# Kernel tuning notes

Hardware: AMD Instinct MI355X
Metric: run time of the kernel (lower is better)

The kernel has to match this reference:

```python
import jax, jax.numpy as jnp
import numpy as np

B, W, LOCAL, GLOBAL = 32, 16, 64, 64
EMB, HIDDEN, OUT, NLAYERS = 256, 512, 64, 3
T = 128  # output_len


def setup_inputs() -> dict:
    key = jax.random.key(0)
    ks = jax.random.split(key, 16)
    s = 0.05
    inp = {
        "z_t": jax.random.normal(ks[0], (B, W, LOCAL), jnp.float32),
        "z_g": jax.random.normal(ks[1], (B, GLOBAL), jnp.float32),
        # embedding: Linear(local+global -> 256, bias=False), torch layout (out,in)
        "w_emb": jax.random.normal(ks[2], (EMB, LOCAL + GLOBAL), jnp.float32) * s,
        # GRU(input_size=1, hidden=256); input is all-zeros so w_ih contributes
        # nothing (only its bias b_ih matters) -> faithfully omit w_ih.
        "gru_w_hh": jax.random.normal(ks[3], (3 * EMB, EMB), jnp.float32) * s,
        "gru_b_ih": jax.random.normal(ks[4], (3 * EMB,), jnp.float32) * s,
        "gru_b_hh": jax.random.normal(ks[5], (3 * EMB,), jnp.float32) * s,
        "mlp_w1": jax.random.normal(ks[6], (HIDDEN, EMB), jnp.float32) * s,
        "mlp_b1": jax.random.normal(ks[7], (HIDDEN,), jnp.float32) * s,
        "mlp_w2": jax.random.normal(ks[8], (HIDDEN, HIDDEN), jnp.float32) * s,
        "mlp_b2": jax.random.normal(ks[9], (HIDDEN,), jnp.float32) * s,
        "mlp_w3": jax.random.normal(ks[10], (HIDDEN, HIDDEN), jnp.float32) * s,
        "mlp_b3": jax.random.normal(ks[11], (HIDDEN,), jnp.float32) * s,
        "mu_w": jax.random.normal(ks[12], (OUT, HIDDEN), jnp.float32) * s,
        "mu_b": jax.random.normal(ks[13], (OUT,), jnp.float32) * s,
        "output_len": T,
    }
    return inp


def _gru_zero_input(h0, w_hh, b_ih, b_hh, length):
    # PyTorch GRU cell with x_t == 0: input-to-hidden term reduces to b_ih.
    b_ir, b_iz, b_in = jnp.split(b_ih, 3)

    def step(h, _):
        gh = h @ w_hh.T + b_hh              # (BW, 3*EMB)
        g_r, g_z, g_n = jnp.split(gh, 3, axis=-1)
        r = jax.nn.sigmoid(b_ir + g_r)
        z = jax.nn.sigmoid(b_iz + g_z)
        n = jnp.tanh(b_in + r * g_n)
        h_new = (1.0 - z) * n + z * h
        return h_new, h_new

    _, hs = jax.lax.scan(step, h0, None, length=length)
    return hs  # (T, BW, EMB)


def reference(z_t, z_g, w_emb, gru_w_hh, gru_b_ih, gru_b_hh,
              mlp_w1, mlp_b1, mlp_w2, mlp_b2, mlp_w3, mlp_b3,
              mu_w, mu_b, output_len):
    b, nw, _ = z_t.shape
    z = jnp.concatenate(
        [z_t, jnp.broadcast_to(z_g[:, None, :], (b, nw, z_g.shape[-1]))], axis=-1)
    emb = z @ w_emb.T                        # (B, W, EMB)
    h0 = emb.reshape(b * nw, -1)             # (BW, EMB) initial hidden state

    hs = _gru_zero_input(h0, gru_w_hh, gru_b_ih, gru_b_hh, output_len)
    h_t = jnp.transpose(hs, (1, 0, 2))       # (BW, T, EMB), batch_first

    # MLP: Linear+ELU (Dropout p=0.05 is identity in eval)
    h = jax.nn.elu(h_t @ mlp_w1.T + mlp_b1)
    h = jax.nn.elu(h @ mlp_w2.T + mlp_b2)
    h = jax.nn.elu(h @ mlp_w3.T + mlp_b3)
    x_mean = h @ mu_w.T + mu_b               # (BW, T, OUT)
    return x_mean.reshape(b, nw * output_len, -1)
```

## Files before the change

### kernel.cpp

```cpp
#include <hip/hip_runtime.h>
#include <hip/hip_bf16.h>


typedef __bf16 bf16_t;
typedef __bf16 bf16x2 __attribute__((ext_vector_type(2)));
typedef __bf16 bf16x4 __attribute__((ext_vector_type(4)));
typedef __bf16 bf16x8 __attribute__((ext_vector_type(8)));
typedef float f32x4 __attribute__((ext_vector_type(4)));

#define MFMA16(a, b, c) __builtin_amdgcn_mfma_f32_16x16x32_bf16(a, b, c, 0, 0, 0)

#define EMB 256
#define TSTEPS 128
#define OUTD 64

#define HS_OFF   0u
#define H0_OFF   33554432u
#define WHH_OFF  34078720u
#define W1_OFF   34471936u
#define W2_OFF   34734080u
#define W3_OFF   35258368u
#define MUW_OFF  35782656u

__device__ __forceinline__ float rcpf(float x){ return __builtin_amdgcn_rcpf(x); }
__device__ __forceinline__ void lds_barrier() {
  asm volatile("s_waitcnt lgkmcnt(0)\n\ts_barrier" ::: "memory");
}
__device__ __forceinline__ float eluf(float x) {
  return (x > 0.f) ? x : (__expf(x) - 1.f);
}

template<int KC>
__device__ __forceinline__ void conv_frag(
    const float* __restrict__ src, bf16_t* __restrict__ dst,
    int NK, int g, int G)
{
  const int K = KC * 128;
  for (int i = g; i < NK; i += G) {
    const int e    = i & 7;
    const int lane = (i >> 3) & 63;
    const int kk   = (i >> 9) & 3;
    const int rem  = i >> 11;
    const int kc   = rem & (KC - 1);
    const int nt   = rem / KC;
    const int l15  = lane & 15, quad = lane >> 4;
    dst[i] = (bf16_t)src[(size_t)(nt * 16 + l15) * K + kc * 128 + kk * 32 + quad * 8 + e];
  }
}

__global__ __launch_bounds__(256) void convert_kernel(
    const float* __restrict__ whh, const float* __restrict__ w1,
    const float* __restrict__ w2, const float* __restrict__ w3,
    const float* __restrict__ muw, char* __restrict__ ws)
{
  const int g = blockIdx.x * 256 + threadIdx.x;
  const int G = gridDim.x * 256;
  bf16_t* d;
  d = (bf16_t*)(ws + WHH_OFF); for (int i = g; i < 196608; i += G) d[i] = (bf16_t)whh[i];
  conv_frag<2>(w1,  (bf16_t*)(ws + W1_OFF),  131072, g, G);
  conv_frag<4>(w2,  (bf16_t*)(ws + W2_OFF),  262144, g, G);
  conv_frag<4>(w3,  (bf16_t*)(ws + W3_OFF),  262144, g, G);
  conv_frag<4>(muw, (bf16_t*)(ws + MUW_OFF), 32768,  g, G);
}

__global__ __launch_bounds__(256) void emb_kernel(
    const float* __restrict__ z_t, const float* __restrict__ z_g,
    const float* __restrict__ w_emb, float* __restrict__ h0)
{
  __shared__ float zrow[128];
  const int bw = blockIdx.x, tid = threadIdx.x;
  if (tid < 128)
    zrow[tid] = (tid < 64) ? z_t[bw * 64 + tid] : z_g[(bw >> 4) * 64 + (tid - 64)];
  __syncthreads();
  const float4* wp = reinterpret_cast<const float4*>(w_emb + (size_t)tid * 128);
  float s = 0.f;
#pragma unroll
  for (int k4 = 0; k4 < 32; ++k4) {
    const float4 w = wp[k4];
    s += zrow[k4 * 4 + 0] * w.x + zrow[k4 * 4 + 1] * w.y
       + zrow[k4 * 4 + 2] * w.z + zrow[k4 * 4 + 3] * w.w;
  }
  h0[(size_t)bw * 256 + tid] = s;
}

__global__ __launch_bounds__(512, 2) void gru_kernel(
    const float* __restrict__ h0, const bf16_t* __restrict__ w_hh,
    const float* __restrict__ b_ih, const float* __restrict__ b_hh,
    bf16_t* __restrict__ hs)
{
  __shared__ __align__(16) bf16_t h16[2][16][264];

  const int tid  = threadIdx.x;
  const int wv   = tid >> 6;
  const int lane = tid & 63;
  const int l15  = lane & 15;
  const int quad = lane >> 4;
  const int bw0  = blockIdx.x * 4;
  const int cA   = wv * 32 + l15;

  bf16x8 wf[6][8];
#pragma unroll
  for (int g = 0; g < 3; ++g)
#pragma unroll
    for (int s = 0; s < 2; ++s) {
      const int n = g * 256 + cA + s * 16;
#pragma unroll
      for (int kk = 0; kk < 8; ++kk)
        wf[g * 2 + s][kk] = *reinterpret_cast<const bf16x8*>(
            w_hh + (size_t)n * 256 + kk * 32 + quad * 8);
    }

  float br[2], bz[2], bin[2], bhn[2], hm[2];
#pragma unroll
  for (int s = 0; s < 2; ++s) {
    const int c = cA + s * 16;
    br[s]  = b_ih[c]       + b_hh[c];
    bz[s]  = b_ih[256 + c] + b_hh[256 + c];
    bin[s] = b_ih[512 + c];
    bhn[s] = b_hh[512 + c];
    hm[s]  = h0[(size_t)(bw0 + quad) * 256 + c];
  }

  {
    bf16x8 zv;
#pragma unroll
    for (int e = 0; e < 8; ++e) zv[e] = (bf16_t)0.f;
    for (int i = tid; i < 1056; i += 512)
      reinterpret_cast<bf16x8*>(h16)[i] = zv;
  }
  __syncthreads();
#pragma unroll
  for (int s = 0; s < 2; ++s)
    h16[0][quad * 4][cA + s * 16] = (bf16_t)hm[s];
  __syncthreads();

  bf16_t* hsp = hs + ((size_t)(bw0 + quad) * TSTEPS) * EMB + cA;

#pragma unroll 1
  for (int t = 0; t < TSTEPS; ++t) {
    const bf16_t (*hr)[264] = h16[t & 1];
    bf16_t (*hw)[264] = h16[(t & 1) ^ 1];

    f32x4 acc[6] = {};
#pragma unroll
    for (int kk = 0; kk < 8; ++kk) {
      const bf16x8 a = *reinterpret_cast<const bf16x8*>(&hr[l15][kk * 32 + quad * 8]);
#pragma unroll
      for (int ct = 0; ct < 6; ++ct)
        acc[ct] = MFMA16(a, wf[ct][kk], acc[ct]);
    }

#pragma unroll
    for (int s = 0; s < 2; ++s) {
      const float gr = acc[s][0]     + br[s];
      const float gz = acc[2 + s][0] + bz[s];
      const float gn = acc[4 + s][0] + bhn[s];
      const float rr = rcpf(1.f + __expf(-gr));
      const float zz = rcpf(1.f + __expf(-gz));
      const float pre = bin[s] + rr * gn;
      const float nn = 1.f - 2.f * rcpf(__expf(2.f * pre) + 1.f);
      hm[s] = nn + zz * (hm[s] - nn);
      const bf16_t nh = (bf16_t)hm[s];
      hw[quad * 4][cA + s * 16] = nh;
      hsp[(size_t)t * EMB + s * 16] = nh;
    }
    lds_barrier();
  }
}

template<int KC>
__device__ __forceinline__ void mlp_layer(
    const bf16_t* __restrict__ Wf, const float* __restrict__ bias,
    bf16_t (*act)[520], int wv, int lane, int l15, int quad)
{
  constexpr int NIT = KC * 4;
  f32x4 acc[8][4] = {};
  bf16x8 wf[2][8];

#pragma unroll
  for (int ct = 0; ct < 8; ++ct)
    wf[0][ct] = *reinterpret_cast<const bf16x8*>(
        Wf + (((size_t)(wv * 8 + ct) * KC) << 11) + lane * 8);

#pragma unroll
  for (int it = 0; it < NIT; ++it) {
    const int cur = it & 1, nxt = cur ^ 1;
    if (it + 1 < NIT) {
      const int kc1 = (it + 1) >> 2, kk1 = (it + 1) & 3;
#pragma unroll
      for (int ct = 0; ct < 8; ++ct)
        wf[nxt][ct] = *reinterpret_cast<const bf16x8*>(
            Wf + ((((size_t)(wv * 8 + ct) * KC + kc1) * 4 + kk1) << 9) + lane * 8);
    }
    const int kc = it >> 2, kk = it & 3;
    bf16x8 a8[4];
#pragma unroll
    for (int mt = 0; mt < 4; ++mt)
      a8[mt] = *reinterpret_cast<const bf16x8*>(
          &act[mt * 16 + l15][kc * 128 + kk * 32 + quad * 8]);
#pragma unroll
    for (int mt = 0; mt < 4; ++mt)
#pragma unroll
      for (int ct = 0; ct < 8; ++ct)
        acc[ct][mt] = MFMA16(wf[cur][ct], a8[mt], acc[ct][mt]);
  }

  __syncthreads();
#pragma unroll
  for (int ct = 0; ct < 8; ++ct) {
    const int nb = (wv * 8 + ct) * 16 + quad * 4;
    const float4 b4 = *reinterpret_cast<const float4*>(bias + nb);
#pragma unroll
    for (int mt = 0; mt < 4; ++mt) {
      bf16x4 v;
      v[0] = (bf16_t)eluf(acc[ct][mt][0] + b4.x);
      v[1] = (bf16_t)eluf(acc[ct][mt][1] + b4.y);
      v[2] = (bf16_t)eluf(acc[ct][mt][2] + b4.z);
      v[3] = (bf16_t)eluf(acc[ct][mt][3] + b4.w);
      *reinterpret_cast<bf16x4*>(&act[mt * 16 + l15][nb]) = v;
    }
  }
  __syncthreads();
}

__global__ __launch_bounds__(256, 2) void mlp_kernel(
    const bf16_t* __restrict__ hs,
    const bf16_t* __restrict__ w1, const float* __restrict__ b1,
    const bf16_t* __restrict__ w2, const float* __restrict__ b2,
    const bf16_t* __restrict__ w3, const float* __restrict__ b3,
    const bf16_t* __restrict__ muw, const float* __restrict__ mub,
    float* __restrict__ out)
{
  __shared__ __align__(16) bf16_t act[64][520];

  const int tid  = threadIdx.x;
  const int wv   = tid >> 6;
  const int lane = tid & 63;
  const int l15  = lane & 15;
  const int quad = lane >> 4;
  const size_t r0 = (size_t)blockIdx.x * 64;

  for (int v = tid; v < 64 * 32; v += 256) {
    const int rr = v >> 5, cc = v & 31;
    bf16x8 x = *reinterpret_cast<const bf16x8*>(hs + (r0 + rr) * EMB + cc * 8);
    *reinterpret_cast<bf16x8*>(&act[rr][cc * 8]) = x;
  }
  __syncthreads();

  mlp_layer<2>(w1, b1, act, wv, lane, l15, quad);
  mlp_layer<4>(w2, b2, act, wv, lane, l15, quad);
  mlp_layer<4>(w3, b3, act, wv, lane, l15, quad);

  f32x4 macc[4] = {};
#pragma unroll
  for (int it = 0; it < 16; ++it) {
    const int kc = it >> 2, kk = it & 3;
    bf16x8 wfm = *reinterpret_cast<const bf16x8*>(
        muw + ((((size_t)wv * 4 + kc) * 4 + kk) << 9) + lane * 8);
#pragma unroll
    for (int i = 0; i < 4; ++i) {
      bf16x8 a = *reinterpret_cast<const bf16x8*>(
          &act[i * 16 + l15][kc * 128 + kk * 32 + quad * 8]);
      macc[i] = MFMA16(wfm, a, macc[i]);
    }
  }
  const int nb = wv * 16 + quad * 4;
  const float4 mb4 = *reinterpret_cast<const float4*>(mub + nb);
#pragma unroll
  for (int i = 0; i < 4; ++i) {
    float4 o;
    o.x = macc[i][0] + mb4.x;
    o.y = macc[i][1] + mb4.y;
    o.z = macc[i][2] + mb4.z;
    o.w = macc[i][3] + mb4.w;
    *reinterpret_cast<float4*>(out + (r0 + i * 16 + l15) * OUTD + nb) = o;
  }
}

extern "C" void kernel_launch(void* const* d_in, const int* in_sizes, int n_in,
                              void* d_out, int out_size, void* d_ws, size_t ws_size,
                              hipStream_t stream) {
  char* ws = (char*)d_ws;

  convert_kernel<<<256, 256, 0, stream>>>(
      (const float*)d_in[3], (const float*)d_in[6], (const float*)d_in[8],
      (const float*)d_in[10], (const float*)d_in[12], ws);

  emb_kernel<<<512, 256, 0, stream>>>(
      (const float*)d_in[0], (const float*)d_in[1], (const float*)d_in[2],
      (float*)(ws + H0_OFF));

  gru_kernel<<<128, 512, 0, stream>>>(
      (const float*)(ws + H0_OFF), (const bf16_t*)(ws + WHH_OFF),
      (const float*)d_in[4], (const float*)d_in[5],
      (bf16_t*)(ws + HS_OFF));

  mlp_kernel<<<1024, 256, 0, stream>>>(
      (const bf16_t*)(ws + HS_OFF),
      (const bf16_t*)(ws + W1_OFF), (const float*)d_in[7],
      (const bf16_t*)(ws + W2_OFF), (const float*)d_in[9],
      (const bf16_t*)(ws + W3_OFF), (const float*)d_in[11],
      (const bf16_t*)(ws + MUW_OFF), (const float*)d_in[13],
      (float*)d_out);
}
```

Measured before the change: 334.3 us.

## Fuse embedding and weight conversion kernels, vectorize conversion, pad GRU LDS rows

Merges the embedding and weight-conversion kernels into one launch: the first 512 blocks compute the embedding and the remaining 256 convert weights. Conversion now handles eight elements per thread with float4 loads and bf16x8 stores instead of scalar element copies. The GRU shared-memory row pitch grows from 264 to 272 elements to change the LDS bank mapping. The output projection swaps its MFMA operands and writes scalar outputs instead of float4, which may reduce store coalescing.

After: 322.7 us. 1.04x faster.

```diff
diff --git a/kernel.cpp b/kernel.cpp
--- a/kernel.cpp
+++ b/kernel.cpp
@@ -29,58 +29,67 @@
 __device__ __forceinline__ float eluf(float x) {
   return (x > 0.f) ? x : (__expf(x) - 1.f);
 }
-
-template<int KC>
-__device__ __forceinline__ void conv_frag(
+__device__ __forceinline__ bf16x8 cvt8(const float* __restrict__ s) {
+  const float4 a = *reinterpret_cast<const float4*>(s);
+  const float4 b = *reinterpret_cast<const float4*>(s + 4);
+  bf16x8 v;
+  v[0] = (bf16_t)a.x; v[1] = (bf16_t)a.y; v[2] = (bf16_t)a.z; v[3] = (bf16_t)a.w;
+  v[4] = (bf16_t)b.x; v[5] = (bf16_t)b.y; v[6] = (bf16_t)b.z; v[7] = (bf16_t)b.w;
+  return v;
+}
+
+template<int KC, int LOGKC>
+__device__ __forceinline__ void conv_frag8(
     const float* __restrict__ src, bf16_t* __restrict__ dst,
-    int NK, int g, int G)
+    int NK8, int g, int G)
 {
   const int K = KC * 128;
-  for (int i = g; i < NK; i += G) {
-    const int e    = i & 7;
-    const int lane = (i >> 3) & 63;
-    const int kk   = (i >> 9) & 3;
-    const int rem  = i >> 11;
+  for (int i8 = g; i8 < NK8; i8 += G) {
+    const int l15  = i8 & 15;
+    const int quad = (i8 >> 4) & 3;
+    const int kk   = (i8 >> 6) & 3;
+    const int rem  = i8 >> 8;
     const int kc   = rem & (KC - 1);
-    const int nt   = rem / KC;
-    const int l15  = lane & 15, quad = lane >> 4;
-    dst[i] = (bf16_t)src[(size_t)(nt * 16 + l15) * K + kc * 128 + kk * 32 + quad * 8 + e];
-  }
-}
-
-__global__ __launch_bounds__(256) void convert_kernel(
+    const int nt   = rem >> LOGKC;
+    *reinterpret_cast<bf16x8*>(dst + (size_t)i8 * 8) =
+        cvt8(src + (size_t)(nt * 16 + l15) * K + kc * 128 + kk * 32 + quad * 8);
+  }
+}
+
+__global__ __launch_bounds__(256) void ce_kernel(
+    const float* __restrict__ z_t, const float* __restrict__ z_g,
+    const float* __restrict__ w_emb, float* __restrict__ h0,
     const float* __restrict__ whh, const float* __restrict__ w1,
     const float* __restrict__ w2, const float* __restrict__ w3,
     const float* __restrict__ muw, char* __restrict__ ws)
 {
-  const int g = blockIdx.x * 256 + threadIdx.x;
-  const int G = gridDim.x * 256;
-  bf16_t* d;
-  d = (bf16_t*)(ws + WHH_OFF); for (int i = g; i < 196608; i += G) d[i] = (bf16_t)whh[i];
-  conv_frag<2>(w1,  (bf16_t*)(ws + W1_OFF),  131072, g, G);
-  conv_frag<4>(w2,  (bf16_t*)(ws + W2_OFF),  262144, g, G);
-  conv_frag<4>(w3,  (bf16_t*)(ws + W3_OFF),  262144, g, G);
-  conv_frag<4>(muw, (bf16_t*)(ws + MUW_OFF), 32768,  g, G);
-}
-
-__global__ __launch_bounds__(256) void emb_kernel(
-    const float* __restrict__ z_t, const float* __restrict__ z_g,
-    const float* __restrict__ w_emb, float* __restrict__ h0)
-{
-  __shared__ float zrow[128];
-  const int bw = blockIdx.x, tid = threadIdx.x;
-  if (tid < 128)
-    zrow[tid] = (tid < 64) ? z_t[bw * 64 + tid] : z_g[(bw >> 4) * 64 + (tid - 64)];
-  __syncthreads();
-  const float4* wp = reinterpret_cast<const float4*>(w_emb + (size_t)tid * 128);
-  float s = 0.f;
-#pragma unroll
-  for (int k4 = 0; k4 < 32; ++k4) {
-    const float4 w = wp[k4];
-    s += zrow[k4 * 4 + 0] * w.x + zrow[k4 * 4 + 1] * w.y
-       + zrow[k4 * 4 + 2] * w.z + zrow[k4 * 4 + 3] * w.w;
-  }
-  h0[(size_t)bw * 256 + tid] = s;
+  const int tid = threadIdx.x;
+  if (blockIdx.x < 512) {
+    __shared__ float zrow[128];
+    const int bw = blockIdx.x;
+    if (tid < 128)
+      zrow[tid] = (tid < 64) ? z_t[bw * 64 + tid] : z_g[(bw >> 4) * 64 + (tid - 64)];
+    __syncthreads();
+    const float4* wp = reinterpret_cast<const float4*>(w_emb + (size_t)tid * 128);
+    float s = 0.f;
+#pragma unroll
+    for (int k4 = 0; k4 < 32; ++k4) {
+      const float4 w = wp[k4];
+      s += zrow[k4 * 4 + 0] * w.x + zrow[k4 * 4 + 1] * w.y
+         + zrow[k4 * 4 + 2] * w.z + zrow[k4 * 4 + 3] * w.w;
+    }
+    h0[(size_t)bw * 256 + tid] = s;
+  } else {
+    const int g = (blockIdx.x - 512) * 256 + tid;
+    const int G = 256 * 256;
+    bf16_t* d = (bf16_t*)(ws + WHH_OFF);
+    for (int i8 = g; i8 < 24576; i8 += G)
+      *reinterpret_cast<bf16x8*>(d + (size_t)i8 * 8) = cvt8(whh + (size_t)i8 * 8);
+    conv_frag8<2, 1>(w1,  (bf16_t*)(ws + W1_OFF),  16384, g, G);
+    conv_frag8<4, 2>(w2,  (bf16_t*)(ws + W2_OFF),  32768, g, G);
+    conv_frag8<4, 2>(w3,  (bf16_t*)(ws + W3_OFF),  32768, g, G);
+    conv_frag8<4, 2>(muw, (bf16_t*)(ws + MUW_OFF),  4096, g, G);
+  }
 }
 
 __global__ __launch_bounds__(512, 2) void gru_kernel(
@@ -88,7 +97,7 @@
     const float* __restrict__ b_ih, const float* __restrict__ b_hh,
     bf16_t* __restrict__ hs)
 {
-  __shared__ __align__(16) bf16_t h16[2][16][264];
+  __shared__ __align__(16) bf16_t h16[2][16][272];
 
   const int tid  = threadIdx.x;
   const int wv   = tid >> 6;
@@ -125,7 +134,7 @@
     bf16x8 zv;
 #pragma unroll
     for (int e = 0; e < 8; ++e) zv[e] = (bf16_t)0.f;
-    for (int i = tid; i < 1056; i += 512)
+    for (int i = tid; i < 1088; i += 512)
       reinterpret_cast<bf16x8*>(h16)[i] = zv;
   }
   __syncthreads();
@@ -138,8 +147,8 @@
 
 #pragma unroll 1
   for (int t = 0; t < TSTEPS; ++t) {
-    const bf16_t (*hr)[264] = h16[t & 1];
-    bf16_t (*hw)[264] = h16[(t & 1) ^ 1];
+    const bf16_t (*hr)[272] = h16[t & 1];
+    bf16_t (*hw)[272] = h16[(t & 1) ^ 1];
 
     f32x4 acc[6] = {};
 #pragma unroll
@@ -252,6 +261,7 @@
   mlp_layer<4>(w3, b3, act, wv, lane, l15, quad);
 
   f32x4 macc[4] = {};
+  const int n = wv * 16 + l15;
 #pragma unroll
   for (int it = 0; it < 16; ++it) {
     const int kc = it >> 2, kk = it & 3;
@@ -261,20 +271,15 @@
     for (int i = 0; i < 4; ++i) {
       bf16x8 a = *reinterpret_cast<const bf16x8*>(
           &act[i * 16 + l15][kc * 128 + kk * 32 + quad * 8]);
-      macc[i] = MFMA16(wfm, a, macc[i]);
-    }
-  }
-  const int nb = wv * 16 + quad * 4;
-  const float4 mb4 = *reinterpret_cast<const float4*>(mub + nb);
-#pragma unroll
-  for (int i = 0; i < 4; ++i) {
-    float4 o;
-    o.x = macc[i][0] + mb4.x;
-    o.y = macc[i][1] + mb4.y;
-    o.z = macc[i][2] + mb4.z;
-    o.w = macc[i][3] + mb4.w;
-    *reinterpret_cast<float4*>(out + (r0 + i * 16 + l15) * OUTD + nb) = o;
-  }
+      macc[i] = MFMA16(a, wfm, macc[i]);
+    }
+  }
+  const float mb = mub[n];
+#pragma unroll
+  for (int i = 0; i < 4; ++i)
+#pragma unroll
+    for (int r = 0; r < 4; ++r)
+      out[(r0 + i * 16 + quad * 4 + r) * OUTD + n] = macc[i][r] + mb;
 }
 
 extern "C" void kernel_launch(void* const* d_in, const int* in_sizes, int n_in,
@@ -282,13 +287,11 @@
                               hipStream_t stream) {
   char* ws = (char*)d_ws;
 
-  convert_kernel<<<256, 256, 0, stream>>>(
+  ce_kernel<<<768, 256, 0, stream>>>(
+      (const float*)d_in[0], (const float*)d_in[1], (const float*)d_in[2],
+      (float*)(ws + H0_OFF),
       (const float*)d_in[3], (const float*)d_in[6], (const float*)d_in[8],
       (const float*)d_in[10], (const float*)d_in[12], ws);
-
-  emb_kernel<<<512, 256, 0, stream>>>(
-      (const float*)d_in[0], (const float*)d_in[1], (const float*)d_in[2],
-      (float*)(ws + H0_OFF));
 
   gru_kernel<<<128, 512, 0, stream>>>(
       (const float*)(ws + H0_OFF), (const bf16_t*)(ws + WHH_OFF),
```
